# Performance work log

Hardware: AMD Instinct MI355X
Metric: run time of the kernel (lower is better)

## Reference

```python
import jax, jax.numpy as jnp
import numpy as np

L = 12      # n_layers
C = 768     # n_embd = dim = dim_att
H = 12      # heads
N = 64      # head_size_a
FF = 2688   # dim_ffn = int(768*3.5//32*32)
P = 2       # patch_size
INCH = 4
IMG = 32
NCLS = 1000
FREQ = 256
HC = C // 2  # conv stem channels (dim//2)
B = 32
D_MIX = 32
D_DEC = 64
LNX_EPS = 1e-5 * 8.0 ** 2  # GroupNorm eps with head_size_divisor=8


def _ln(x, w=None, b=None, eps=1e-5):
    m = x.mean(-1, keepdims=True)
    v = x.var(-1, keepdims=True)
    xh = (x - m) * jax.lax.rsqrt(v + eps)
    if w is not None:
        xh = xh * w + b
    return xh


def _shift(x):  # RWKV token shift: prepend zero row, drop last
    return jnp.pad(x, ((0, 0), (1, 0), (0, 0)))[:, :-1]


def _gn_img(x, w, b, groups=32, eps=1e-5):
    Bb, Ch, Hh, Ww = x.shape
    xg = x.reshape(Bb, groups, Ch // groups, Hh, Ww)
    m = xg.mean((2, 3, 4), keepdims=True)
    v = xg.var((2, 3, 4), keepdims=True)
    xg = (xg - m) * jax.lax.rsqrt(v + eps)
    return xg.reshape(Bb, Ch, Hh, Ww) * w[None, :, None, None] + b[None, :, None, None]


def _conv5(x, w, b):
    y = jax.lax.conv_general_dilated(x, w, (1, 1), ((2, 2), (2, 2)),
                                     dimension_numbers=('NCHW', 'OIHW', 'NCHW'))
    return y + b[None, :, None, None]


def _wkv(r, k, v, w, u):
    # r,k,v,w: (B,T,H,N); u: (H,N). S[b,h,i,j]: key i -> value j.
    def step(S, inp):
        rt, kt, vt, wt = inp  # each (B,H,N)
        kv = kt[..., :, None] * vt[..., None, :]           # (B,H,N,N)
        y = jnp.einsum('bhi,bhij->bhj', rt, S + u[None, :, :, None] * kv)
        S = wt[..., :, None] * S + kv
        return S, y
    S0 = jnp.zeros((r.shape[0], H, N, N), r.dtype)
    seq = tuple(jnp.moveaxis(a, 1, 0) for a in (r, k, v, w))
    _, ys = jax.lax.scan(step, S0, seq)
    return jnp.moveaxis(ys, 0, 1)  # (B,T,H,N)


def _timemix(x, p):
    Bb, Tt, _ = x.shape
    xx = _shift(x) - x
    xxx = x + xx * p['maa'][0]
    mix = jnp.tanh(xxx @ p['tm_w1']).reshape(Bb, Tt, 5, D_MIX)
    m = jnp.einsum('btfd,fdc->fbtc', mix, p['tm_w2'])  # (5,B,T,C): mw,mk,mv,mr,mg
    xw = x + xx * (p['maa'][1] + m[0])
    xk = x + xx * (p['maa'][2] + m[1])
    xv = x + xx * (p['maa'][3] + m[2])
    xr = x + xx * (p['maa'][4] + m[3])
    xg = x + xx * (p['maa'][5] + m[4])
    r = (xr @ p['r_w'].T).reshape(Bb, Tt, H, N)
    k = (xk @ p['k_w'].T).reshape(Bb, Tt, H, N)
    v = (xv @ p['v_w'].T).reshape(Bb, Tt, H, N)
    g = jax.nn.silu(xg @ p['g_w'].T)
    ww = p['td'] + jnp.tanh(xw @ p['td_w1']) @ p['td_w2']
    w = jnp.exp(-jnp.exp(ww)).reshape(Bb, Tt, H, N)
    y = _wkv(r, k, v, w, p['faaaa'])  # (B,T,H,N)
    mn = y.mean(-1, keepdims=True)
    vr = y.var(-1, keepdims=True)
    y = ((y - mn) * jax.lax.rsqrt(vr + LNX_EPS)).reshape(Bb, Tt, C) * p['lnx_w'] + p['lnx_b']
    return (y * g) @ p['o_w'].T


def _chanmix(x, p):
    xx = _shift(x) - x
    xk = x + xx * p['fmaa'][0]
    xr = x + xx * p['fmaa'][1]
    k = jnp.square(jax.nn.relu(xk @ p['fk_w'].T))
    return jax.nn.sigmoid(xr @ p['fr_w'].T) * (k @ p['fv_w'].T)


def _forward(x, t, y, c1_w, c1_b, gn1_w, gn1_b, c2_w, c2_b, gn2_w, gn2_b,
             xe_w, xe_b, te_w1, te_b1, te_w2, te_b2, y_tab, ln0_w, ln0_b,
             ln1_w, ln1_b, ln2_w, ln2_b, att_maa, tm_w1, tm_w2, td, td_w1,
             td_w2, faaaa, r_w, k_w, v_w, o_w, g_w, lnx_w, lnx_b, ffn_maa,
             fk_w, fr_w, fv_w, ada_w, ada_b, fl_ada_w, fl_ada_b, fl_w, fl_b):
    Bb = x.shape[0]
    h = jax.nn.silu(_conv5(x, c1_w, c1_b))
    h = _gn_img(h, gn1_w, gn1_b)
    h = jax.nn.silu(_conv5(h, c2_w, c2_b))
    h = _gn_img(h, gn2_w, gn2_b)
    # patchify: (B,HC,IMG,IMG) -> (B,T,P*P*HC)
    G = IMG // P
    h = h.reshape(Bb, HC, G, P, G, P).transpose(0, 2, 4, 1, 3, 5).reshape(Bb, G * G, HC * P * P)
    xs = h @ xe_w.T + xe_b
    # timestep embedding
    half = FREQ // 2
    freqs = jnp.exp(-jnp.log(10000.0) * jnp.arange(half, dtype=jnp.float32) / half)
    ang = t[:, None] * freqs[None]
    temb = jnp.concatenate([jnp.cos(ang), jnp.sin(ang)], -1)
    temb = jax.nn.silu(temb @ te_w1.T + te_b1) @ te_w2.T + te_b2
    c = temb + y_tab[y]  # adaln_input (B,C)
    for l in range(L):
        ada = jax.nn.silu(c) @ ada_w[l].T + ada_b[l]
        sm, scm, gm, sp, scp, gp = jnp.split(ada, 6, axis=1)
        if l == 0:
            xs = _ln(xs, ln0_w, ln0_b)
        p = dict(maa=att_maa[l], tm_w1=tm_w1[l], tm_w2=tm_w2[l], td=td[l],
                 td_w1=td_w1[l], td_w2=td_w2[l], faaaa=faaaa[l], r_w=r_w[l],
                 k_w=k_w[l], v_w=v_w[l], o_w=o_w[l], g_w=g_w[l], lnx_w=lnx_w[l],
                 lnx_b=lnx_b[l], fmaa=ffn_maa[l], fk_w=fk_w[l], fr_w=fr_w[l],
                 fv_w=fv_w[l])
        hmod = _ln(xs, ln1_w[l], ln1_b[l]) * (1 + scm[:, None, :]) + sm[:, None, :]
        xs = xs + gm[:, None, :] * _timemix(hmod, p)
        hmod = _ln(xs, ln2_w[l], ln2_b[l]) * (1 + scp[:, None, :]) + sp[:, None, :]
        xs = xs + gp[:, None, :] * _chanmix(hmod, p)
    ada = jax.nn.silu(c) @ fl_ada_w.T + fl_ada_b
    sh, sc = jnp.split(ada, 2, axis=1)
    out = (_ln(xs, eps=1e-6) * (1 + sc[:, None, :]) + sh[:, None, :]) @ fl_w.T + fl_b
    G = IMG // P
    out = out.reshape(Bb, G, G, P, P, INCH)
    out = jnp.einsum('nhwpqc->nchpwq', out).reshape(Bb, INCH, IMG, IMG)
    return out


def setup_inputs() -> dict:
    key = jax.random.key(0)
    ks = iter(jax.random.split(key, 64))
    def rn(shape, s=0.02):
        return (jax.random.normal(next(ks), shape) * s).astype(jnp.float32)
    inp = {}
    inp['x'] = jax.random.normal(next(ks), (B, INCH, IMG, IMG), jnp.float32)
    inp['t'] = jax.random.uniform(next(ks), (B,), jnp.float32) * 1000.0
    inp['y'] = jax.random.randint(next(ks), (B,), 0, NCLS)
    inp['c1_w'] = rn((HC, INCH, 5, 5), 0.05); inp['c1_b'] = jnp.zeros(HC)
    inp['gn1_w'] = jnp.ones(HC); inp['gn1_b'] = jnp.zeros(HC)
    inp['c2_w'] = rn((HC, HC, 5, 5), 0.02); inp['c2_b'] = jnp.zeros(HC)
    inp['gn2_w'] = jnp.ones(HC); inp['gn2_b'] = jnp.zeros(HC)
    inp['xe_w'] = rn((C, P * P * HC)); inp['xe_b'] = jnp.zeros(C)
    inp['te_w1'] = rn((C, FREQ)); inp['te_b1'] = jnp.zeros(C)
    inp['te_w2'] = rn((C, C)); inp['te_b2'] = jnp.zeros(C)
    inp['y_tab'] = rn((NCLS + 1, C))
    inp['ln0_w'] = jnp.ones(C); inp['ln0_b'] = jnp.zeros(C)
    inp['ln1_w'] = jnp.ones((L, C)); inp['ln1_b'] = jnp.zeros((L, C))
    inp['ln2_w'] = jnp.ones((L, C)); inp['ln2_b'] = jnp.zeros((L, C))
    inp['att_maa'] = jax.random.uniform(next(ks), (L, 6, C), jnp.float32)
    inp['tm_w1'] = rn((L, C, 5 * D_MIX), 0.01)
    inp['tm_w2'] = rn((L, 5, D_MIX, C), 0.01)
    inp['td'] = rn((L, C), 0.5) - 3.0
    inp['td_w1'] = rn((L, C, D_DEC), 0.01)
    inp['td_w2'] = rn((L, D_DEC, C), 0.01)
    inp['faaaa'] = rn((L, H, N), 0.1)
    for nm in ('r_w', 'k_w', 'v_w', 'o_w', 'g_w'):
        inp[nm] = rn((L, C, C))
    inp['lnx_w'] = jnp.ones((L, C)); inp['lnx_b'] = jnp.zeros((L, C))
    inp['ffn_maa'] = jax.random.uniform(next(ks), (L, 2, C), jnp.float32)
    inp['fk_w'] = rn((L, FF, C)); inp['fr_w'] = rn((L, C, C)); inp['fv_w'] = rn((L, C, FF))
    inp['ada_w'] = rn((L, 6 * C, C)); inp['ada_b'] = jnp.zeros((L, 6 * C))
    inp['fl_ada_w'] = rn((2 * C, C)); inp['fl_ada_b'] = jnp.zeros(2 * C)
    inp['fl_w'] = rn((P * P * INCH, C)); inp['fl_b'] = jnp.zeros(P * P * INCH)
    return inp


def reference(x, t, y, c1_w, c1_b, gn1_w, gn1_b, c2_w, c2_b, gn2_w, gn2_b,
              xe_w, xe_b, te_w1, te_b1, te_w2, te_b2, y_tab, ln0_w, ln0_b,
              ln1_w, ln1_b, ln2_w, ln2_b, att_maa, tm_w1, tm_w2, td, td_w1,
              td_w2, faaaa, r_w, k_w, v_w, o_w, g_w, lnx_w, lnx_b, ffn_maa,
              fk_w, fr_w, fv_w, ada_w, ada_b, fl_ada_w, fl_ada_b, fl_w, fl_b):
    return _forward(x, t, y, c1_w, c1_b, gn1_w, gn1_b, c2_w, c2_b, gn2_w, gn2_b,
                    xe_w, xe_b, te_w1, te_b1, te_w2, te_b2, y_tab, ln0_w, ln0_b,
                    ln1_w, ln1_b, ln2_w, ln2_b, att_maa, tm_w1, tm_w2, td, td_w1,
                    td_w2, faaaa, r_w, k_w, v_w, o_w, g_w, lnx_w, lnx_b, ffn_maa,
                    fk_w, fr_w, fv_w, ada_w, ada_b, fl_ada_w, fl_ada_b, fl_w, fl_b)
```

## Files before the change

kernel.cpp:

```cpp
#include <hip/hip_runtime.h>
#include <math.h>


typedef short  s16x8 __attribute__((ext_vector_type(8)));
typedef float  f32x4 __attribute__((ext_vector_type(4)));
typedef __attribute__((address_space(1))) const void as1_cv;
typedef __attribute__((address_space(3))) void as3_v;

#define GLDS16(gp, lp) __builtin_amdgcn_global_load_lds( \
    (as1_cv*)(unsigned long long)(const void*)(gp), \
    (as3_v*)(unsigned int)(unsigned long long)(void*)(lp), 16, 0, 0)

static __device__ __forceinline__ float sigf(float x){ return 1.f/(1.f+expf(-x)); }
static __device__ __forceinline__ unsigned short f2b(float x){
  unsigned int u = __builtin_bit_cast(unsigned int, x);
  unsigned int r = (u + 0x7FFFu + ((u >> 16) & 1u)) >> 16;
  return (unsigned short)r;
}
static __device__ __forceinline__ float b2f(unsigned short h){
  unsigned int u = ((unsigned int)h)<<16; return __builtin_bit_cast(float,u);
}

static const size_t O_XS    = 0ull;
static const size_t O_HMOD  = 6291456ull;
static const size_t O_ADA   = 12582912ull;
static const size_t O_FLA   = 14352384ull;
static const size_t O_T2    = 14401536ull;
static const size_t O_SC    = 14426112ull;
static const size_t O_TI    = 14450688ull;
static const size_t O_T1    = 14458880ull;
static const size_t O_ST1   = 14483456ull;
static const size_t O_ST2   = 14485504ull;
static const size_t O_XEW16 = 14487552ull;
static const size_t O_WL16  = 15077376ull;
static const size_t O_BIG   = 19107840ull;
static const size_t L_XW    = 0ull;
static const size_t L_XX    = 6291456ull;
static const size_t L_XXX   = 12582912ull;
static const size_t L_KB    = 18874368ull;
static const size_t L_VB    = 25165824ull;
static const size_t L_GB    = 31457280ull;
static const size_t L_WD    = 37748736ull;
static const size_t L_MIXB  = 50331648ull;
static const size_t L_WT    = 51642368ull;
static const size_t L_XK16  = 52166656ull;
static const size_t L_XV16  = 55312384ull;
static const size_t L_XR16  = 58458112ull;
static const size_t L_XG16  = 61603840ull;
static const size_t L_GNH16 = 64749568ull;
static const size_t L_KBIG16= 67895296ull;
static const size_t S_IMG1  = 0ull;
static const size_t S_IMG2  = 12582912ull;
static const size_t S_PAD16 = 25165824ull;
static const size_t S_WTAP16= 33128448ull;
static const size_t S_PM16  = 34971648ull;

enum { EPI_NONE=0, EPI_SILU=1 };

template<int EPI, bool TB>
__global__ __launch_bounds__(256) void gemm_k(
    const float* __restrict__ A, const float* __restrict__ B,
    float* __restrict__ C, const float* __restrict__ bias,
    int M, int N, int K)
{
  __shared__ __align__(16) float As[16][68];
  __shared__ __align__(16) float Bs[16][68];
  const int tid = threadIdx.x;
  const int tx = tid & 15, ty = tid >> 4;
  const int row0 = blockIdx.y * 64, col0 = blockIdx.x * 64;
  const int lr = tid >> 2;
  const int lk = (tid & 3) << 2;
  float acc[4][4] = {};
  for (int k0 = 0; k0 < K; k0 += 16) {
    {
      int gr = row0 + lr;
      float4 v = make_float4(0.f,0.f,0.f,0.f);
      if (gr < M) v = *reinterpret_cast<const float4*>(A + (size_t)gr*K + (k0 + lk));
      As[lk+0][lr]=v.x; As[lk+1][lr]=v.y; As[lk+2][lr]=v.z; As[lk+3][lr]=v.w;
    }
    if (TB) {
      int gr = col0 + lr;
      float4 v = make_float4(0.f,0.f,0.f,0.f);
      if (gr < N) v = *reinterpret_cast<const float4*>(B + (size_t)gr*K + (k0 + lk));
      Bs[lk+0][lr]=v.x; Bs[lk+1][lr]=v.y; Bs[lk+2][lr]=v.z; Bs[lk+3][lr]=v.w;
    } else {
      int kr = tid >> 4;
      int gc = col0 + ((tid & 15) << 2);
      float4 v = make_float4(0.f,0.f,0.f,0.f);
      if (gc < N) v = *reinterpret_cast<const float4*>(B + (size_t)(k0+kr)*N + gc);
      Bs[kr][((tid&15)<<2)+0]=v.x; Bs[kr][((tid&15)<<2)+1]=v.y;
      Bs[kr][((tid&15)<<2)+2]=v.z; Bs[kr][((tid&15)<<2)+3]=v.w;
    }
    __syncthreads();
    #pragma unroll
    for (int kk=0;kk<16;kk++){
      const float4 a4 = *reinterpret_cast<const float4*>(&As[kk][ty<<2]);
      const float4 b4 = *reinterpret_cast<const float4*>(&Bs[kk][tx<<2]);
      const float av[4]={a4.x,a4.y,a4.z,a4.w};
      const float bv[4]={b4.x,b4.y,b4.z,b4.w};
      #pragma unroll
      for (int i=0;i<4;i++)
        #pragma unroll
        for (int j=0;j<4;j++)
          acc[i][j]=fmaf(av[i],bv[j],acc[i][j]);
    }
    __syncthreads();
  }
  #pragma unroll
  for (int i=0;i<4;i++){
    const int r = row0 + (ty<<2) + i;
    if (r >= M) break;
    #pragma unroll
    for (int j=0;j<4;j++){
      const int c = col0 + (tx<<2) + j;
      if (c >= N) break;
      float v = acc[i][j];
      if (bias) v += bias[c];
      const size_t idx = (size_t)r*N + c;
      if (EPI==EPI_NONE)        C[idx]=v;
      else if (EPI==EPI_SILU)   C[idx]=v*sigf(v);
    }
  }
}

#define GEMM(EPI,TB,A,B,C,bias,M,N,K) \
  gemm_k<EPI,TB><<<dim3(((N)+63)/64,((M)+63)/64),dim3(256),0,stream>>>((A),(B),(C),(bias),(M),(N),(K))

enum { BEPI_F32=0, BEPI_BIAS_F32, BEPI_SILU_F32, BEPI_SIG_F32, BEPI_RELU2_BF16,
       BEPI_RES_GM, BEPI_RES_GP16, BEPI_TANH_BF16, BEPI_WDEC_F32 };

template<int EPI>
__global__ __launch_bounds__(256) void bgemm_k(
    const unsigned short* __restrict__ A, const unsigned short* __restrict__ B,
    void* __restrict__ Cv, const float* __restrict__ bias,
    const float* __restrict__ p1, const void* __restrict__ p2, int pstride,
    int M, int N, int K)
{
  __shared__ __align__(16) unsigned short As[128][64];
  __shared__ __align__(16) unsigned short Bs[128][64];
  const int tid = threadIdx.x;
  const int w = tid >> 6, lane = tid & 63;
  const int row0 = blockIdx.y * 128, col0 = blockIdx.x * 128;
  const int wr = w >> 1, wc = w & 1;
  const int l15 = lane & 15, l4 = lane >> 4;
  const int kkc = ((lane & 7) ^ (lane >> 3)) * 8;
  f32x4 acc[4][4] = {};
  for (int k0 = 0; k0 < K; k0 += 64) {
    #pragma unroll
    for (int i = 0; i < 4; i++) {
      const int rb = i*32 + w*8;
      const int r  = rb + (lane >> 3);
      GLDS16(A + (size_t)(row0 + r)*K + k0 + kkc, &As[rb][0]);
      GLDS16(B + (size_t)(col0 + r)*K + k0 + kkc, &Bs[rb][0]);
    }
    __syncthreads();
    #pragma unroll
    for (int ks = 0; ks < 2; ks++) {
      s16x8 af[4], bf[4];
      #pragma unroll
      for (int m = 0; m < 4; m++) {
        const int r = wr*64 + m*16 + l15;
        const int sl = (ks*4 + l4) ^ (r & 7);
        af[m] = *reinterpret_cast<const s16x8*>(&As[r][sl*8]);
      }
      #pragma unroll
      for (int n = 0; n < 4; n++) {
        const int r = wc*64 + n*16 + l15;
        const int sl = (ks*4 + l4) ^ (r & 7);
        bf[n] = *reinterpret_cast<const s16x8*>(&Bs[r][sl*8]);
      }
      #pragma unroll
      for (int m = 0; m < 4; m++)
        #pragma unroll
        for (int n = 0; n < 4; n++)
          acc[m][n] = __builtin_amdgcn_mfma_f32_16x16x32_bf16(af[m], bf[n], acc[m][n], 0, 0, 0);
    }
    __syncthreads();
  }
  float* Cf = (float*)Cv; unsigned short* Ch = (unsigned short*)Cv;
  const unsigned short* p2h = (const unsigned short*)p2;
  #pragma unroll
  for (int m = 0; m < 4; m++) {
    const int rbase = row0 + wr*64 + m*16 + (l4<<2);
    #pragma unroll
    for (int n = 0; n < 4; n++) {
      const int c = col0 + wc*64 + n*16 + l15;
      if (c >= N) continue;
      #pragma unroll
      for (int q = 0; q < 4; q++) {
        const int r = rbase + q;
        const int bb = r >> 8;
        float v = acc[m][n][q];
        const size_t idx = (size_t)r*N + c;
        if (EPI==BEPI_F32)            Cf[idx] = v;
        else if (EPI==BEPI_BIAS_F32)  Cf[idx] = v + bias[c];
        else if (EPI==BEPI_SILU_F32)  Cf[idx] = v*sigf(v);
        else if (EPI==BEPI_SIG_F32)   Cf[idx] = sigf(v);
        else if (EPI==BEPI_RELU2_BF16){ float t=fmaxf(v,0.f); Ch[idx] = f2b(t*t); }
        else if (EPI==BEPI_RES_GM)    Cf[idx] += p1[(size_t)bb*pstride + c]*v;
        else if (EPI==BEPI_RES_GP16)  Cf[idx] += p1[(size_t)bb*pstride + c]*(b2f(p2h[idx])*v);
        else if (EPI==BEPI_TANH_BF16) Ch[idx] = f2b(tanhf(v));
        else if (EPI==BEPI_WDEC_F32)  Cf[idx] = expf(-expf(v + p1[c]));
      }
    }
  }
}

#define BGEMM(EPI,A16,B16,Cp,bias,p1,p2,ps,M,N,K) \
  bgemm_k<EPI><<<dim3(((N)+127)/128,(M)/128),dim3(256),0,stream>>>( \
    (const unsigned short*)(A16),(const unsigned short*)(B16),(void*)(Cp),(bias),(p1),(p2),(ps),(M),(N),(K))

struct BGrp { const unsigned short* A; const unsigned short* B; void* C;
              int epi; int N; int gx; };
struct BGrp4 { BGrp g[4]; };

__global__ __launch_bounds__(256) void bgemm_grp_k(BGrp4 G, int M, int K)
{
  const BGrp gr = G.g[blockIdx.z];
  if ((int)blockIdx.x >= gr.gx) return;
  __shared__ __align__(16) unsigned short As[128][64];
  __shared__ __align__(16) unsigned short Bs[128][64];
  const int tid = threadIdx.x;
  const int w = tid >> 6, lane = tid & 63;
  const int row0 = blockIdx.y * 128, col0 = blockIdx.x * 128;
  const int wr = w >> 1, wc = w & 1;
  const int l15 = lane & 15, l4 = lane >> 4;
  const int kkc = ((lane & 7) ^ (lane >> 3)) * 8;
  const int N = gr.N;
  f32x4 acc[4][4] = {};
  for (int k0 = 0; k0 < K; k0 += 64) {
    #pragma unroll
    for (int i = 0; i < 4; i++) {
      const int rb = i*32 + w*8;
      const int r  = rb + (lane >> 3);
      GLDS16(gr.A + (size_t)(row0 + r)*K + k0 + kkc, &As[rb][0]);
      GLDS16(gr.B + (size_t)(col0 + r)*K + k0 + kkc, &Bs[rb][0]);
    }
    __syncthreads();
    #pragma unroll
    for (int ks = 0; ks < 2; ks++) {
      s16x8 af[4], bf[4];
      #pragma unroll
      for (int m = 0; m < 4; m++) {
        const int r = wr*64 + m*16 + l15;
        const int sl = (ks*4 + l4) ^ (r & 7);
        af[m] = *reinterpret_cast<const s16x8*>(&As[r][sl*8]);
      }
      #pragma unroll
      for (int n = 0; n < 4; n++) {
        const int r = wc*64 + n*16 + l15;
        const int sl = (ks*4 + l4) ^ (r & 7);
        bf[n] = *reinterpret_cast<const s16x8*>(&Bs[r][sl*8]);
      }
      #pragma unroll
      for (int m = 0; m < 4; m++)
        #pragma unroll
        for (int n = 0; n < 4; n++)
          acc[m][n] = __builtin_amdgcn_mfma_f32_16x16x32_bf16(af[m], bf[n], acc[m][n], 0, 0, 0);
    }
    __syncthreads();
  }
  float* Cf = (float*)gr.C; unsigned short* Ch = (unsigned short*)gr.C;
  #pragma unroll
  for (int m = 0; m < 4; m++) {
    const int rbase = row0 + wr*64 + m*16 + (l4<<2);
    #pragma unroll
    for (int n = 0; n < 4; n++) {
      const int c = col0 + wc*64 + n*16 + l15;
      #pragma unroll
      for (int q = 0; q < 4; q++) {
        const int r = rbase + q;
        float v = acc[m][n][q];
        const size_t idx = (size_t)r*N + c;
        switch (gr.epi) {
          case 0: Cf[idx] = v; break;
          case 1: Cf[idx] = v*sigf(v); break;
          case 3: { float t=fmaxf(v,0.f); Ch[idx] = f2b(t*t); } break;
          case 4: Ch[idx] = f2b(v); break;
          case 5: Ch[idx] = f2b(v*sigf(v)); break;
          default: Ch[idx] = f2b(sigf(v)); break;
        }
      }
    }
  }
}

__global__ __launch_bounds__(256) void conv1_k(
    const float* __restrict__ x, const float* __restrict__ w,
    const float* __restrict__ bias, float* __restrict__ out)
{
  const int blk = blockIdx.x; const int bb = blk / 384; const int oc = blk % 384;
  __shared__ __align__(16) float sIn[4*1296];
  __shared__ __align__(16) float sW[100];
// ... 127 lines not shown
            af[m] = *reinterpret_cast<const s16x8*>(&As[r][sl*8]);
          }
          #pragma unroll
          for (int n = 0; n < 4; n++) {
            const int r = wc*64 + n*16 + l15;
            const int sl = (ks*4 + l4) ^ (r & 7);
            bf[n] = *reinterpret_cast<const s16x8*>(&Bs[r][sl*8]);
          }
          #pragma unroll
          for (int m = 0; m < 4; m++)
            #pragma unroll
            for (int n = 0; n < 4; n++)
              acc[m][n] = __builtin_amdgcn_mfma_f32_16x16x32_bf16(af[m], bf[n], acc[m][n], 0, 0, 0);
        }
        __syncthreads();
      }
    }
  }
  #pragma unroll
  for (int m = 0; m < 4; m++) {
    #pragma unroll
    for (int n = 0; n < 4; n++) {
      const int oc = oc0 + wc*64 + n*16 + l15;
      const float bv = bias[oc];
      #pragma unroll
      for (int q = 0; q < 4; q++) {
        const int p = wr*64 + m*16 + (l4<<2) + q;
        const int py = p >> 5, px = p & 31;
        float v = acc[m][n][q] + bv;
        out[((size_t)b*1024 + (y0+py)*32 + px)*384 + oc] = f2b(v*sigf(v));
      }
    }
  }
}

__global__ __launch_bounds__(256) void gn_stats_nhwc_k(
    const unsigned short* __restrict__ h, float* __restrict__ stats)
{
  const int b = blockIdx.x >> 5, g = blockIdx.x & 31;
  const int tid = threadIdx.x;
  float s=0.f, s2=0.f;
  for (int idx=tid; idx<12288; idx+=256){
    int p = idx/12, c = idx - p*12;
    float v = b2f(h[((size_t)b*1024+p)*384 + g*12 + c]);
    s+=v; s2=fmaf(v,v,s2);
  }
  #pragma unroll
  for (int mask=32; mask>=1; mask>>=1){ s += __shfl_xor(s,mask); s2 += __shfl_xor(s2,mask); }
  __shared__ float ps[8];
  if ((tid&63)==0){ ps[tid>>6]=s; ps[4+(tid>>6)]=s2; }
  __syncthreads();
  if (tid==0){
    s = ps[0]+ps[1]+ps[2]+ps[3]; s2 = ps[4]+ps[5]+ps[6]+ps[7];
    float mean = s*(1.f/12288.f);
    float var  = s2*(1.f/12288.f) - mean*mean;
    stats[(b*32+g)*2] = mean; stats[(b*32+g)*2+1] = rsqrtf(var + 1e-5f);
  }
}

__global__ void patchify_gn_k(const unsigned short* __restrict__ h, const float* __restrict__ stats,
                              const float* __restrict__ w, const float* __restrict__ bgn,
                              unsigned short* __restrict__ pm)
{
  int idx = blockIdx.x*256 + threadIdx.x;
  int row = idx/1536, f = idx - row*1536;
  int c = f>>2; int p=(f>>1)&1; int q=f&1;
  int bb=row>>8; int tok=row&255; int gh=tok>>4, gw=tok&15;
  int pix = (gh*2+p)*32 + gw*2+q;
  int g = c / 12;
  float mean = stats[(bb*32+g)*2], rstd = stats[(bb*32+g)*2+1];
  float v = (b2f(h[((size_t)bb*1024 + pix)*384 + c]) - mean)*rstd*w[c] + bgn[c];
  pm[idx] = f2b(v);
}

__global__ void temb_in_k(const float* __restrict__ t, float* __restrict__ out)
{
  int bb = blockIdx.x; int i = threadIdx.x;
  float fr = expf(-logf(10000.f) * (float)i / 128.f);
  float ang = t[bb]*fr;
  out[bb*256+i]     = cosf(ang);
  out[bb*256+128+i] = sinf(ang);
}

__global__ void siluc_k(const float* __restrict__ t2, const float* __restrict__ ytab,
                        const int* __restrict__ y, float* __restrict__ sc)
{
  int bb = blockIdx.x; int tid = threadIdx.x;
  int cls = y[bb];
  for (int c=tid; c<768; c+=256){
    float v = t2[bb*768+c] + ytab[(size_t)cls*768+c];
    sc[bb*768+c] = v*sigf(v);
  }
}

__global__ __launch_bounds__(256) void ln_mod_k(
    const float* __restrict__ in, float* __restrict__ out,
    const float* __restrict__ w, const float* __restrict__ b,
    const float* __restrict__ mod, int mstride, int sh_off, int sc_off, float eps)
{
  const int m = blockIdx.x; const int tid = threadIdx.x;
  const size_t base = (size_t)m*768;
  float v0=in[base+tid], v1=in[base+tid+256], v2=in[base+tid+512];
  float s = v0+v1+v2;
  float s2 = fmaf(v0,v0,fmaf(v1,v1,v2*v2));
  #pragma unroll
  for (int mask=32; mask>=1; mask>>=1){ s += __shfl_xor(s,mask); s2 += __shfl_xor(s2,mask); }
  __shared__ float ps[8];
  if ((tid&63)==0){ ps[tid>>6]=s; ps[4+(tid>>6)]=s2; }
  __syncthreads();
  s = ps[0]+ps[1]+ps[2]+ps[3]; s2 = ps[4]+ps[5]+ps[6]+ps[7];
  const float mean = s*(1.f/768.f);
  const float var  = s2*(1.f/768.f) - mean*mean;
  const float rstd = rsqrtf(var + eps);
  const int bb = m >> 8;
  #pragma unroll
  for (int k=0;k<3;k++){
    const int c = tid + k*256;
    float v = (k==0)?v0:((k==1)?v1:v2);
    float xh = (v-mean)*rstd;
    if (w) xh = fmaf(xh, w[c], b[c]);
    if (mod){
      float scv = mod[(size_t)bb*mstride + sc_off + c];
      float shv = mod[(size_t)bb*mstride + sh_off + c];
      xh = fmaf(xh, 1.f+scv, shv);
    }
    out[base+c] = xh;
  }
}

__global__ __launch_bounds__(256) void ln_shift_tm_k(
    const float* __restrict__ xs, const float* __restrict__ w, const float* __restrict__ b,
    const float* __restrict__ mod, const float* __restrict__ maa0,
    unsigned short* __restrict__ hmod16, unsigned short* __restrict__ xx16,
    unsigned short* __restrict__ xxx16)
{
  const int m = blockIdx.x, tid = threadIdx.x;
  const size_t base = (size_t)m*768;
  const int t = m & 255, bb = m >> 8;
  float c0=xs[base+tid], c1=xs[base+tid+256], c2=xs[base+tid+512];
  float p0=0.f,p1=0.f,p2=0.f;
  if (t) { p0=xs[base-768+tid]; p1=xs[base-512+tid]; p2=xs[base-256+tid]; }
  float sc_=c0+c1+c2, sc2=fmaf(c0,c0,fmaf(c1,c1,c2*c2));
  float sp_=p0+p1+p2, sp2=fmaf(p0,p0,fmaf(p1,p1,p2*p2));
  #pragma unroll
  for (int mask=32; mask>=1; mask>>=1){
    sc_+=__shfl_xor(sc_,mask); sc2+=__shfl_xor(sc2,mask);
    sp_+=__shfl_xor(sp_,mask); sp2+=__shfl_xor(sp2,mask);
  }
  __shared__ float ps[16];
  if ((tid&63)==0){ int wv=tid>>6; ps[wv]=sc_; ps[4+wv]=sc2; ps[8+wv]=sp_; ps[12+wv]=sp2; }
  __syncthreads();
  sc_=ps[0]+ps[1]+ps[2]+ps[3]; sc2=ps[4]+ps[5]+ps[6]+ps[7];
  sp_=ps[8]+ps[9]+ps[10]+ps[11]; sp2=ps[12]+ps[13]+ps[14]+ps[15];
  const float mc = sc_*(1.f/768.f), rc = rsqrtf(sc2*(1.f/768.f)-mc*mc + 1e-5f);
  const float mp = sp_*(1.f/768.f), rp = rsqrtf(sp2*(1.f/768.f)-mp*mp + 1e-5f);
  #pragma unroll
  for (int k=0;k<3;k++){
    const int c = tid + k*256;
    const float scv = mod[(size_t)bb*55296 + 768 + c];
    const float shv = mod[(size_t)bb*55296 + c];
    float cv = (k==0)?c0:((k==1)?c1:c2);
    float h = fmaf((cv-mc)*rc, w[c], b[c]);
    h = fmaf(h, 1.f+scv, shv);
    float pv = 0.f;
    if (t) {
      float pk = (k==0)?p0:((k==1)?p1:p2);
      pv = fmaf((pk-mp)*rp, w[c], b[c]);
      pv = fmaf(pv, 1.f+scv, shv);
    }
    const float d = pv - h;
    hmod16[base+c] = f2b(h);
    xx16[base+c] = f2b(d);
    xxx16[base+c] = f2b(fmaf(d, maa0[c], h));
  }
// ... 240 lines not shown
            const int srow = n*16 + l15;
            s16x8 kf = *reinterpret_cast<const s16x8*>(&kk16[srow][(((kt*4+l4)^(srow&7))<<3)]);
            Aac[m][n] = __builtin_amdgcn_mfma_f32_16x16x32_bf16(rrf[m][kt], kf, Aac[m][n], 0,0,0);
          }
      #pragma unroll
      for (int m=0;m<2;m++)
        #pragma unroll
        for (int n=0;n<2;n++)
          #pragma unroll
          for (int q=0;q<4;q++){
            const int t = m*16 + l4*4 + q;
            const int s = n*16 + l15;
            float av = Aac[m][n][q];
            av = (s < t) ? av : ((s == t) ? diag[t] : 0.f);
            A16[t][(((s>>3)^(t&3))<<3) + (s&7)] = f2b(av);
          }
    }
    #pragma unroll
    for (int m=0;m<4;m++)
      #pragma unroll
      for (int q=0;q<4;q++){
        const int i = m*16 + l4*4 + q;
        S16T[jj][(((i>>3)^(jj&7))<<3) + (i&7)] = f2b(S_acc[m][q]);
      }
    __syncthreads();
    #pragma unroll
    for (int m=0;m<2;m++){
      const int row = m*16 + l15;
      s16x8 af = *reinterpret_cast<const s16x8*>(&A16[row][((l4^(row&3))<<3)]);
      Y[m] = __builtin_amdgcn_mfma_f32_16x16x32_bf16(af, vtf, Y[m], 0,0,0);
    }
    #pragma unroll
    for (int m=0;m<2;m++)
      #pragma unroll
      for (int q=0;q<4;q++){
        float s1 = Y[m][q], s2 = s1*s1;
        #pragma unroll
        for (int mask=8; mask>=1; mask>>=1){ s1 += __shfl_xor(s1,mask); s2 += __shfl_xor(s2,mask); }
        if (l15==0){ const int t = m*16 + l4*4 + q; ypsum[t][w]=s1; ypsq[t][w]=s2; }
      }
    __syncthreads();
    #pragma unroll
    for (int m=0;m<2;m++)
      #pragma unroll
      for (int q=0;q<4;q++){
        const int t = m*16 + l4*4 + q;
        float s1 = ypsum[t][0]+ypsum[t][1]+ypsum[t][2]+ypsum[t][3];
        float s2 = ypsq[t][0]+ypsq[t][1]+ypsq[t][2]+ypsq[t][3];
        float mean = s1*(1.f/64.f);
        float var  = s2*(1.f/64.f) - mean*mean;
        float xh = (Y[m][q]-mean)*rsqrtf(var + 6.4e-4f);
        float o = fmaf(xh, lw, lb) * b2f(g16s[t][jj]);
        out16[gb + (size_t)(c*32+t)*768 + jj] = f2b(o);
      }
    if (c < 7) {
      __syncthreads();
      WKV_STAGE();
      __syncthreads();
    }
  }
#undef WKV_LOADC
#undef WKV_STAGE
}

__global__ void unpatch_k(const float* __restrict__ po, float* __restrict__ out)
{
  int idx = blockIdx.x*256 + threadIdx.x;
  int xq=idx&31; int yy=(idx>>5)&31; int ch=(idx>>10)&3; int bb=idx>>12;
  int gh=yy>>1, p=yy&1, gw=xq>>1, q=xq&1;
  out[idx] = po[((size_t)(bb*256+gh*16+gw))*16 + p*8+q*4+ch];
}

__global__ void f2b_k(const float* __restrict__ s, unsigned short* __restrict__ d)
{
  size_t i = ((size_t)blockIdx.x*256 + threadIdx.x)*8;
  float4 a = *reinterpret_cast<const float4*>(s+i);
  float4 b = *reinterpret_cast<const float4*>(s+i+4);
  s16x8 o;
  o[0]=(short)f2b(a.x); o[1]=(short)f2b(a.y); o[2]=(short)f2b(a.z); o[3]=(short)f2b(a.w);
  o[4]=(short)f2b(b.x); o[5]=(short)f2b(b.y); o[6]=(short)f2b(b.z); o[7]=(short)f2b(b.w);
  *reinterpret_cast<s16x8*>(d + i) = o;
}

__global__ void f2bw_layer_k(
    const float* __restrict__ r_, const float* __restrict__ k_, const float* __restrict__ v_,
    const float* __restrict__ o_, const float* __restrict__ g_, const float* __restrict__ fr_,
    const float* __restrict__ fk_, const float* __restrict__ fv_,
    const float* __restrict__ tm1, const float* __restrict__ td1, const float* __restrict__ td2,
    unsigned short* __restrict__ dst)
{
  if (blockIdx.x < 3744) {
    size_t i = ((size_t)blockIdx.x*256 + threadIdx.x)*8;
    const float* s; size_t off;
    if (i < 3538944) {
      unsigned seg = (unsigned)(i / 589824u); off = i - (size_t)seg*589824u;
      s = seg==0?r_:seg==1?k_:seg==2?v_:seg==3?o_:seg==4?g_:fr_;
    } else if (i < 5603328) { s = fk_; off = i - 3538944; }
    else                    { s = fv_; off = i - 5603328; }
    float4 a = *reinterpret_cast<const float4*>(s+off);
    float4 b = *reinterpret_cast<const float4*>(s+off+4);
    s16x8 o;
    o[0]=(short)f2b(a.x); o[1]=(short)f2b(a.y); o[2]=(short)f2b(a.z); o[3]=(short)f2b(a.w);
    o[4]=(short)f2b(b.x); o[5]=(short)f2b(b.y); o[6]=(short)f2b(b.z); o[7]=(short)f2b(b.w);
    *reinterpret_cast<s16x8*>(dst + i) = o;
  } else {
    int idx = (blockIdx.x-3744)*256 + threadIdx.x;
    unsigned short* rp = dst + 7667712;
    if (idx < 196608) {
      int n = idx/768, k = idx - n*768;
      rp[idx] = (n<160) ? f2b(tm1[(size_t)k*160 + n]) : (unsigned short)0;
    } else if (idx < 294912) {
      int i = idx-196608; int n = i/768, k = i - n*768;
      rp[idx] = (n<64) ? f2b(td1[(size_t)k*64 + n]) : (unsigned short)0;
    } else {
      int i = idx-294912; int n = i/64, k = i - n*64;
      rp[idx] = f2b(td2[(size_t)k*768 + n]);
    }
  }
}

extern "C" void kernel_launch(void* const* d_in, const int* in_sizes, int n_in,
                              void* d_out, int out_size, void* d_ws, size_t ws_size,
                              hipStream_t stream)
{
  const float* x_in  = (const float*)d_in[0];
  const float* t_in  = (const float*)d_in[1];
  const int*   y_in  = (const int*)  d_in[2];
  const float* c1w   = (const float*)d_in[3];
  const float* c1b   = (const float*)d_in[4];
  const float* gn1w  = (const float*)d_in[5];
  const float* gn1b  = (const float*)d_in[6];
  const float* c2w   = (const float*)d_in[7];
  const float* c2b   = (const float*)d_in[8];
  const float* gn2w  = (const float*)d_in[9];
  const float* gn2b  = (const float*)d_in[10];
  const float* xew   = (const float*)d_in[11];
  const float* xeb   = (const float*)d_in[12];
  const float* tew1  = (const float*)d_in[13];
  const float* teb1  = (const float*)d_in[14];
  const float* tew2  = (const float*)d_in[15];
  const float* teb2  = (const float*)d_in[16];
  const float* ytab  = (const float*)d_in[17];
  const float* ln0w  = (const float*)d_in[18];
  const float* ln0b  = (const float*)d_in[19];
  const float* ln1w  = (const float*)d_in[20];
  const float* ln1b  = (const float*)d_in[21];
  const float* ln2w  = (const float*)d_in[22];
  const float* ln2b  = (const float*)d_in[23];
  const float* amaa  = (const float*)d_in[24];
  const float* tmw1  = (const float*)d_in[25];
  const float* tmw2  = (const float*)d_in[26];
  const float* tdv   = (const float*)d_in[27];
  const float* tdw1  = (const float*)d_in[28];
  const float* tdw2  = (const float*)d_in[29];
  const float* faa   = (const float*)d_in[30];
  const float* rw    = (const float*)d_in[31];
  const float* kw    = (const float*)d_in[32];
  const float* vw    = (const float*)d_in[33];
  const float* ow    = (const float*)d_in[34];
  const float* gw    = (const float*)d_in[35];
  const float* lnxw  = (const float*)d_in[36];
  const float* lnxb  = (const float*)d_in[37];
  const float* fmaa  = (const float*)d_in[38];
  const float* fkw   = (const float*)d_in[39];
  const float* frw   = (const float*)d_in[40];
  const float* fvw   = (const float*)d_in[41];
  const float* adaw  = (const float*)d_in[42];
  const float* adab  = (const float*)d_in[43];
  const float* flaw  = (const float*)d_in[44];
  const float* flab  = (const float*)d_in[45];
  const float* flw   = (const float*)d_in[46];
  const float* flb   = (const float*)d_in[47];

  float* Wf = (float*)d_ws;
  float* xs   = Wf+O_XS;   float* hmodf = Wf+O_HMOD;
  float* ada  = Wf+O_ADA;  float* fla  = Wf+O_FLA;
  float* t2   = Wf+O_T2;   float* sc   = Wf+O_SC;
  float* ti   = Wf+O_TI;   float* t1   = Wf+O_T1;
  float* st1  = Wf+O_ST1;  float* st2  = Wf+O_ST2;
  unsigned short* xew16 = (unsigned short*)(Wf+O_XEW16);
  unsigned short* wl16  = (unsigned short*)(Wf+O_WL16);
  unsigned short* hmod16 = (unsigned short*)(Wf+O_HMOD);
  float* big = Wf+O_BIG;
  float* wd   = big+L_WD;
  unsigned short* xx16  = (unsigned short*)(big+L_XX);
  unsigned short* rb16  = (unsigned short*)(big+L_XXX);
  unsigned short* kb16  = (unsigned short*)(big+L_KB);
  unsigned short* vb16  = (unsigned short*)(big+L_VB);
  unsigned short* gb16  = (unsigned short*)(big+L_GB);
  unsigned short* xw16  = (unsigned short*)(big+L_XW);
  unsigned short* xxx16 = (unsigned short*)(big+L_XXX);
  unsigned short* mixb16= (unsigned short*)(big+L_MIXB);
  unsigned short* wt16  = (unsigned short*)(big+L_WT);
  unsigned short* xk16 = (unsigned short*)(big+L_XK16);
  unsigned short* xv16 = (unsigned short*)(big+L_XV16);
  unsigned short* xr16 = (unsigned short*)(big+L_XR16);
  unsigned short* xg16 = (unsigned short*)(big+L_XG16);
  unsigned short* gnh16 = (unsigned short*)(big+L_GNH16);
  unsigned short* kbig16 = (unsigned short*)(big+L_KBIG16);
  float* img1 = big+S_IMG1;
  unsigned short* img2_16 = (unsigned short*)(big+S_IMG2);
  unsigned short* pad16  = (unsigned short*)(big+S_PAD16);
  unsigned short* wtap16 = (unsigned short*)(big+S_WTAP16);
  unsigned short* pm16   = (unsigned short*)(big+S_PM16);
  float* pout = big+L_MIXB;
  unsigned short* dr  = wl16;
  unsigned short* dk  = wl16 + 589824;
  unsigned short* dv  = wl16 + 1179648;
  unsigned short* do_ = wl16 + 1769472;
  unsigned short* dg  = wl16 + 2359296;
  unsigned short* dfr = wl16 + 2949120;
  unsigned short* dfk = wl16 + 3538944;
  unsigned short* dfv = wl16 + 5603328;
  unsigned short* dtm1t = wl16 + 7667712;
  unsigned short* dtd1t = wl16 + 7864320;
  unsigned short* dtd2t = wl16 + 7962624;

  conv1_k<<<dim3(32*384),dim3(256),0,stream>>>(x_in, c1w, c1b, img1);
  gn_stats_nchw_k<<<dim3(1024),dim3(256),0,stream>>>(img1, st1);
  zero16_k<<<dim3(7776),dim3(256),0,stream>>>(pad16);
  pad_apply_k<<<dim3(1024),dim3(256),0,stream>>>(img1, st1, gn1w, gn1b, pad16);
  wrepack_k<<<dim3(384),dim3(256),0,stream>>>(c2w, wtap16);
  conv2m_k<<<dim3(768),dim3(256),0,stream>>>(pad16, wtap16, c2b, img2_16);
  gn_stats_nhwc_k<<<dim3(1024),dim3(256),0,stream>>>(img2_16, st2);
  patchify_gn_k<<<dim3(49152),dim3(256),0,stream>>>(img2_16, st2, gn2w, gn2b, pm16);
  f2b_k<<<dim3(576),dim3(256),0,stream>>>(xew, xew16);
  BGEMM(BEPI_BIAS_F32, pm16, xew16, xs, xeb, nullptr,nullptr,0, 8192,768,1536);

  temb_in_k<<<dim3(32),dim3(128),0,stream>>>(t_in, ti);
  GEMM(EPI_SILU,true, ti, tew1, t1, teb1, 32,768,256);
  GEMM(EPI_NONE,true, t1, tew2, t2, teb2, 32,768,768);
  siluc_k<<<dim3(32),dim3(256),0,stream>>>(t2, ytab, y_in, sc);
  GEMM(EPI_NONE,true, sc, adaw, ada, adab, 32,55296,768);
  GEMM(EPI_NONE,true, sc, flaw, fla, flab, 32,1536,768);

  ln_mod_k<<<dim3(8192),dim3(256),0,stream>>>(xs, xs, ln0w, ln0b, nullptr, 0,0,0, 1e-5f);

  for (int l=0; l<12; l++){
    const float* adal = ada + (size_t)l*4608;
    f2bw_layer_k<<<dim3(5088),dim3(256),0,stream>>>(
        rw+(size_t)l*589824, kw+(size_t)l*589824, vw+(size_t)l*589824,
        ow+(size_t)l*589824, gw+(size_t)l*589824, frw+(size_t)l*589824,
        fkw+(size_t)l*2064384, fvw+(size_t)l*2064384,
        tmw1+(size_t)l*122880, tdw1+(size_t)l*49152, tdw2+(size_t)l*49152, wl16);
    ln_shift_tm_k<<<dim3(8192),dim3(256),0,stream>>>(
        xs, ln1w+(size_t)l*768, ln1b+(size_t)l*768, adal, amaa+(size_t)l*4608,
        hmod16, xx16, xxx16);
    BGEMM(BEPI_TANH_BF16, xxx16, dtm1t, mixb16, nullptr,nullptr,nullptr,0, 8192,160,768);
    five_mix_k<<<dim3(512),dim3(256),0,stream>>>(mixb16, tmw2+(size_t)l*122880, hmod16, xx16,
                                                 amaa+(size_t)l*4608+768, xw16,xk16,xv16,xr16,xg16);
    BGEMM(BEPI_TANH_BF16, xw16, dtd1t, wt16, nullptr,nullptr,nullptr,0, 8192,64,768);
    BGEMM(BEPI_WDEC_F32, wt16, dtd2t, wd, nullptr, tdv+(size_t)l*768, nullptr,0, 8192,768,64);
    {
      BGrp4 G;
      G.g[0].A=xr16; G.g[0].B=dr; G.g[0].C=rb16; G.g[0].epi=4; G.g[0].N=768; G.g[0].gx=6;
      G.g[1].A=xk16; G.g[1].B=dk; G.g[1].C=kb16; G.g[1].epi=4; G.g[1].N=768; G.g[1].gx=6;
      G.g[2].A=xv16; G.g[2].B=dv; G.g[2].C=vb16; G.g[2].epi=4; G.g[2].N=768; G.g[2].gx=6;
      G.g[3].A=xg16; G.g[3].B=dg; G.g[3].C=gb16; G.g[3].epi=5; G.g[3].N=768; G.g[3].gx=6;
      bgemm_grp_k<<<dim3(6,64,4),dim3(256),0,stream>>>(G, 8192, 768);
    }
    wkv_k<<<dim3(384),dim3(256),0,stream>>>(rb16, kb16, vb16, wd, gb16, faa+(size_t)l*768,
                                            lnxw+(size_t)l*768, lnxb+(size_t)l*768, gnh16);
    BGEMM(BEPI_RES_GM, gnh16, do_, xs, nullptr, adal+1536, nullptr, 55296, 8192,768,768);
    ln_shift_cm_k<<<dim3(8192),dim3(256),0,stream>>>(
        xs, ln2w+(size_t)l*768, ln2b+(size_t)l*768, adal, fmaa+(size_t)l*1536, xk16, xr16);
    {
      BGrp4 G;
      G.g[0].A=xk16; G.g[0].B=dfk; G.g[0].C=kbig16; G.g[0].epi=3; G.g[0].N=2688; G.g[0].gx=21;
      G.g[1].A=xr16; G.g[1].B=dfr; G.g[1].C=gb16;   G.g[1].epi=7; G.g[1].N=768;  G.g[1].gx=6;
      G.g[2]=G.g[1]; G.g[3]=G.g[1];
      bgemm_grp_k<<<dim3(21,64,2),dim3(256),0,stream>>>(G, 8192, 768);
    }
    BGEMM(BEPI_RES_GP16, kbig16, dfv, xs, nullptr, adal+3840, gb16, 55296, 8192,768,2688);
  }

  ln_mod_k<<<dim3(8192),dim3(256),0,stream>>>(xs, hmodf, nullptr, nullptr, fla, 1536, 0, 768, 1e-6f);
  GEMM(EPI_NONE,true, hmodf, flw, pout, flb, 8192,16,768);
  unpatch_k<<<dim3(512),dim3(256),0,stream>>>(pout, (float*)d_out);
}
```

Baseline: 8.233 ms.

## Move adaLN projection to bf16 MFMA GEMM and batch all-layer weight conversion

The large adaLN modulation GEMM (32x55296x768) and the final-layer modulation GEMM now run on the bf16 MFMA path instead of the scalar fp32 tiled GEMM. The conditioning input is zero-padded to 128 rows and output writes are masked to the 32 real rows. When the workspace is large enough, all 12 layers' weights are converted to bf16 in a single launch instead of one launch per layer. The adaLN weights are now rounded to bf16, which may cost some accuracy, and the 4x row padding wastes MFMA work.

Measured after the change: 8.511 ms. +3.4%, slower.

```diff
diff --git a/kernel.cpp b/kernel.cpp
--- a/kernel.cpp
+++ b/kernel.cpp
@@ -54,6 +54,12 @@
 static const size_t S_PAD16 = 25165824ull;
 static const size_t S_WTAP16= 33128448ull;
 static const size_t S_PM16  = 34971648ull;
+static const size_t C_ADAW16= 0ull;
+static const size_t C_FLAW16= 22000000ull;
+static const size_t C_SC16  = 23000000ull;
+static const size_t O_ALLW  = 98013184ull;
+static const int    WST     = 8011776;
+static const size_t ALLW_FLOATS = 48070656ull;
 
 enum { EPI_NONE=0, EPI_SILU=1 };
 
@@ -134,7 +140,7 @@
     const unsigned short* __restrict__ A, const unsigned short* __restrict__ B,
     void* __restrict__ Cv, const float* __restrict__ bias,
     const float* __restrict__ p1, const void* __restrict__ p2, int pstride,
-    int M, int N, int K)
+    int M, int N, int K, int Mst)
 {
   __shared__ __align__(16) unsigned short As[128][64];
   __shared__ __align__(16) unsigned short Bs[128][64];
@@ -189,6 +195,7 @@
       #pragma unroll
       for (int q = 0; q < 4; q++) {
         const int r = rbase + q;
+        if (r >= Mst) continue;
         const int bb = r >> 8;
         float v = acc[m][n][q];
         const size_t idx = (size_t)r*N + c;
@@ -208,7 +215,10 @@
 
 #define BGEMM(EPI,A16,B16,Cp,bias,p1,p2,ps,M,N,K) \
   bgemm_k<EPI><<<dim3(((N)+127)/128,(M)/128),dim3(256),0,stream>>>( \
-    (const unsigned short*)(A16),(const unsigned short*)(B16),(void*)(Cp),(bias),(p1),(p2),(ps),(M),(N),(K))
+    (const unsigned short*)(A16),(const unsigned short*)(B16),(void*)(Cp),(bias),(p1),(p2),(ps),(M),(N),(K),(M))
+#define BGEMMP(EPI,A16,B16,Cp,bias,M,N,K,MS) \
+  bgemm_k<EPI><<<dim3(((N)+127)/128,(M)/128),dim3(256),0,stream>>>( \
+    (const unsigned short*)(A16),(const unsigned short*)(B16),(void*)(Cp),(bias),nullptr,nullptr,0,(M),(N),(K),(MS))
 
 struct BGrp { const unsigned short* A; const unsigned short* B; void* C;
               int epi; int N; int gx; };
@@ -502,14 +512,18 @@
   out[bb*256+128+i] = sinf(ang);
 }
 
-__global__ void siluc_k(const float* __restrict__ t2, const float* __restrict__ ytab,
-                        const int* __restrict__ y, float* __restrict__ sc)
-{
-  int bb = blockIdx.x; int tid = threadIdx.x;
-  int cls = y[bb];
-  for (int c=tid; c<768; c+=256){
-    float v = t2[bb*768+c] + ytab[(size_t)cls*768+c];
-    sc[bb*768+c] = v*sigf(v);
+__global__ void siluc16_k(const float* __restrict__ t2, const float* __restrict__ ytab,
+                          const int* __restrict__ y, unsigned short* __restrict__ sc16)
+{
+  int row = blockIdx.x; int tid = threadIdx.x;
+  if (row < 32) {
+    int cls = y[row];
+    for (int c=tid; c<768; c+=256){
+      float v = t2[row*768+c] + ytab[(size_t)cls*768+c];
+      sc16[(size_t)row*768+c] = f2b(v*sigf(v));
+    }
+  } else {
+    for (int c=tid; c<768; c+=256) sc16[(size_t)row*768+c] = 0;
   }
 }
 
@@ -916,15 +930,16 @@
   *reinterpret_cast<s16x8*>(d + i) = o;
 }
 
-__global__ void f2bw_layer_k(
-    const float* __restrict__ r_, const float* __restrict__ k_, const float* __restrict__ v_,
-    const float* __restrict__ o_, const float* __restrict__ g_, const float* __restrict__ fr_,
-    const float* __restrict__ fk_, const float* __restrict__ fv_,
-    const float* __restrict__ tm1, const float* __restrict__ td1, const float* __restrict__ td2,
-    unsigned short* __restrict__ dst)
-{
-  if (blockIdx.x < 3744) {
-    size_t i = ((size_t)blockIdx.x*256 + threadIdx.x)*8;
+static __device__ __forceinline__ void f2bw_body(
+    int bx, int tid,
+    const float* r_, const float* k_, const float* v_,
+    const float* o_, const float* g_, const float* fr_,
+    const float* fk_, const float* fv_,
+    const float* tm1, const float* td1, const float* td2,
+    unsigned short* dst)
+{
+  if (bx < 3744) {
+    size_t i = ((size_t)bx*256 + tid)*8;
     const float* s; size_t off;
     if (i < 3538944) {
       unsigned seg = (unsigned)(i / 589824u); off = i - (size_t)seg*589824u;
@@ -938,7 +953,7 @@
     o[4]=(short)f2b(b.x); o[5]=(short)f2b(b.y); o[6]=(short)f2b(b.z); o[7]=(short)f2b(b.w);
     *reinterpret_cast<s16x8*>(dst + i) = o;
   } else {
-    int idx = (blockIdx.x-3744)*256 + threadIdx.x;
+    int idx = (bx-3744)*256 + tid;
     unsigned short* rp = dst + 7667712;
     if (idx < 196608) {
       int n = idx/768, k = idx - n*768;
@@ -951,6 +966,32 @@
       rp[idx] = f2b(td2[(size_t)k*768 + n]);
     }
   }
+}
+
+__global__ void f2bw_layer_k(
+    const float* __restrict__ r_, const float* __restrict__ k_, const float* __restrict__ v_,
+    const float* __restrict__ o_, const float* __restrict__ g_, const float* __restrict__ fr_,
+    const float* __restrict__ fk_, const float* __restrict__ fv_,
+    const float* __restrict__ tm1, const float* __restrict__ td1, const float* __restrict__ td2,
+    unsigned short* __restrict__ dst)
+{
+  f2bw_body(blockIdx.x, threadIdx.x, r_,k_,v_,o_,g_,fr_,fk_,fv_,tm1,td1,td2, dst);
+}
+
+__global__ void f2bw_all_k(
+    const float* __restrict__ r_, const float* __restrict__ k_, const float* __restrict__ v_,
+    const float* __restrict__ o_, const float* __restrict__ g_, const float* __restrict__ fr_,
+    const float* __restrict__ fk_, const float* __restrict__ fv_,
+    const float* __restrict__ tm1, const float* __restrict__ td1, const float* __restrict__ td2,
+    unsigned short* __restrict__ dst_all)
+{
+  const size_t l = blockIdx.y;
+  f2bw_body(blockIdx.x, threadIdx.x,
+            r_ + l*589824, k_ + l*589824, v_ + l*589824,
+            o_ + l*589824, g_ + l*589824, fr_ + l*589824,
+            fk_ + l*2064384, fv_ + l*2064384,
+            tm1 + l*122880, td1 + l*49152, td2 + l*49152,
+            dst_all + l*(size_t)WST);
 }
 
 extern "C" void kernel_launch(void* const* d_in, const int* in_sizes, int n_in,
@@ -1009,7 +1050,7 @@
   float* Wf = (float*)d_ws;
   float* xs   = Wf+O_XS;   float* hmodf = Wf+O_HMOD;
   float* ada  = Wf+O_ADA;  float* fla  = Wf+O_FLA;
-  float* t2   = Wf+O_T2;   float* sc   = Wf+O_SC;
+  float* t2   = Wf+O_T2;
   float* ti   = Wf+O_TI;   float* t1   = Wf+O_T1;
   float* st1  = Wf+O_ST1;  float* st2  = Wf+O_ST2;
   unsigned short* xew16 = (unsigned short*)(Wf+O_XEW16);
@@ -1037,18 +1078,12 @@
   unsigned short* pad16  = (unsigned short*)(big+S_PAD16);
   unsigned short* wtap16 = (unsigned short*)(big+S_WTAP16);
   unsigned short* pm16   = (unsigned short*)(big+S_PM16);
+  unsigned short* adaw16 = (unsigned short*)(big+C_ADAW16);
+  unsigned short* flaw16 = (unsigned short*)(big+C_FLAW16);
+  unsigned short* sc16   = (unsigned short*)(big+C_SC16);
   float* pout = big+L_MIXB;
-  unsigned short* dr  = wl16;
-  unsigned short* dk  = wl16 + 589824;
-  unsigned short* dv  = wl16 + 1179648;
-  unsigned short* do_ = wl16 + 1769472;
-  unsigned short* dg  = wl16 + 2359296;
-  unsigned short* dfr = wl16 + 2949120;
-  unsigned short* dfk = wl16 + 3538944;
-  unsigned short* dfv = wl16 + 5603328;
-  unsigned short* dtm1t = wl16 + 7667712;
-  unsigned short* dtd1t = wl16 + 7864320;
-  unsigned short* dtd2t = wl16 + 7962624;
+  unsigned short* allw = (unsigned short*)(Wf + O_ALLW);
+  const bool big_ws = ws_size >= (size_t)(O_ALLW + ALLW_FLOATS) * 4ull;
 
   conv1_k<<<dim3(32*384),dim3(256),0,stream>>>(x_in, c1w, c1b, img1);
   gn_stats_nchw_k<<<dim3(1024),dim3(256),0,stream>>>(img1, st1);
@@ -1064,19 +1099,40 @@
   temb_in_k<<<dim3(32),dim3(128),0,stream>>>(t_in, ti);
   GEMM(EPI_SILU,true, ti, tew1, t1, teb1, 32,768,256);
   GEMM(EPI_NONE,true, t1, tew2, t2, teb2, 32,768,768);
-  siluc_k<<<dim3(32),dim3(256),0,stream>>>(t2, ytab, y_in, sc);
-  GEMM(EPI_NONE,true, sc, adaw, ada, adab, 32,55296,768);
-  GEMM(EPI_NONE,true, sc, flaw, fla, flab, 32,1536,768);
+  siluc16_k<<<dim3(128),dim3(256),0,stream>>>(t2, ytab, y_in, sc16);
+  f2b_k<<<dim3(20736),dim3(256),0,stream>>>(adaw, adaw16);
+  f2b_k<<<dim3(576),dim3(256),0,stream>>>(flaw, flaw16);
+  BGEMMP(BEPI_BIAS_F32, sc16, adaw16, ada, adab, 128,55296,768, 32);
+  BGEMMP(BEPI_BIAS_F32, sc16, flaw16, fla, flab, 128,1536,768, 32);
+
+  if (big_ws) {
+    f2bw_all_k<<<dim3(5088,12),dim3(256),0,stream>>>(
+        rw, kw, vw, ow, gw, frw, fkw, fvw, tmw1, tdw1, tdw2, allw);
+  }
 
   ln_mod_k<<<dim3(8192),dim3(256),0,stream>>>(xs, xs, ln0w, ln0b, nullptr, 0,0,0, 1e-5f);
 
   for (int l=0; l<12; l++){
     const float* adal = ada + (size_t)l*4608;
-    f2bw_layer_k<<<dim3(5088),dim3(256),0,stream>>>(
-        rw+(size_t)l*589824, kw+(size_t)l*589824, vw+(size_t)l*589824,
-        ow+(size_t)l*589824, gw+(size_t)l*589824, frw+(size_t)l*589824,
-        fkw+(size_t)l*2064384, fvw+(size_t)l*2064384,
-        tmw1+(size_t)l*122880, tdw1+(size_t)l*49152, tdw2+(size_t)l*49152, wl16);
+    unsigned short* wl = big_ws ? (allw + (size_t)l*WST) : wl16;
+    if (!big_ws) {
+      f2bw_layer_k<<<dim3(5088),dim3(256),0,stream>>>(
+          rw+(size_t)l*589824, kw+(size_t)l*589824, vw+(size_t)l*589824,
+          ow+(size_t)l*589824, gw+(size_t)l*589824, frw+(size_t)l*589824,
+          fkw+(size_t)l*2064384, fvw+(size_t)l*2064384,
+          tmw1+(size_t)l*122880, tdw1+(size_t)l*49152, tdw2+(size_t)l*49152, wl16);
+    }
+    unsigned short* dr  = wl;
+    unsigned short* dk  = wl + 589824;
+    unsigned short* dv  = wl + 1179648;
+    unsigned short* do_ = wl + 1769472;
+    unsigned short* dg  = wl + 2359296;
+    unsigned short* dfr = wl + 2949120;
+    unsigned short* dfk = wl + 3538944;
+    unsigned short* dfv = wl + 5603328;
+    unsigned short* dtm1t = wl + 7667712;
+    unsigned short* dtd1t = wl + 7864320;
+    unsigned short* dtd2t = wl + 7962624;
     ln_shift_tm_k<<<dim3(8192),dim3(256),0,stream>>>(
         xs, ln1w+(size_t)l*768, ln1b+(size_t)l*768, adal, amaa+(size_t)l*4608,
         hmod16, xx16, xxx16);
```
